# Kernel optimization log

Hardware: AMD Instinct MI355X
Metric: run time of the kernel (lower is better)

Reference implementation:

```python
import jax, jax.numpy as jnp
import numpy as np

T, V, K = 128, 5023, 16  # time frames, FLAME vertices, max neighbors


def setup_inputs() -> dict:
    key = jax.random.key(0)
    k1, k2, k3, k4 = jax.random.split(key, 4)
    canonical = jax.random.normal(k1, (T, V, 3), dtype=jnp.float32)
    deformed = canonical + 0.1 * jax.random.normal(k2, (T, V, 3), dtype=jnp.float32)
    neighbors = jax.random.randint(k3, (V, K), 0, V)
    neighbors_mask = jax.random.bernoulli(k4, 0.8, (V, K))
    return {
        "canonical_vertices": canonical,
        "deformed_vertices": deformed,
        "neighbors": neighbors,
        "neighbors_mask": neighbors_mask,
    }


def _matrix_to_quaternion(M):
    """Rotation matrix [..., 3, 3] -> quaternion [..., 4] (w, x, y, z).
    Standard numerically-robust 4-candidate selection (pytorch3d style)."""
    m00, m01, m02 = M[..., 0, 0], M[..., 0, 1], M[..., 0, 2]
    m10, m11, m12 = M[..., 1, 0], M[..., 1, 1], M[..., 1, 2]
    m20, m21, m22 = M[..., 2, 0], M[..., 2, 1], M[..., 2, 2]
    q_abs = jnp.sqrt(jnp.clip(jnp.stack([
        1.0 + m00 + m11 + m22,
        1.0 + m00 - m11 - m22,
        1.0 - m00 + m11 - m22,
        1.0 - m00 - m11 + m22,
    ], axis=-1), 0.0, None))
    quat_by_rijk = jnp.stack([
        jnp.stack([q_abs[..., 0] ** 2, m21 - m12, m02 - m20, m10 - m01], -1),
        jnp.stack([m21 - m12, q_abs[..., 1] ** 2, m01 + m10, m02 + m20], -1),
        jnp.stack([m02 - m20, m10 + m01, q_abs[..., 2] ** 2, m12 + m21], -1),
        jnp.stack([m10 - m01, m20 + m02, m21 + m12, q_abs[..., 3] ** 2], -1),
    ], axis=-2)  # [..., 4, 4]
    floor = jnp.asarray(0.1, M.dtype)
    quat_candidates = quat_by_rijk / (2.0 * jnp.maximum(q_abs[..., None], floor))
    one_hot = jax.nn.one_hot(jnp.argmax(q_abs, axis=-1), 4, dtype=M.dtype)
    return jnp.sum(quat_candidates * one_hot[..., None], axis=-2)


def reference(canonical_vertices, deformed_vertices, neighbors, neighbors_mask):
    dtype = canonical_vertices.dtype
    maskf = neighbors_mask[..., None].astype(dtype)  # [V, K, 1]
    # gather neighbor positions, zeroing padded slots (matches torch code)
    p = canonical_vertices[:, neighbors, :] * maskf  # [T, V, K, 3]
    q = deformed_vertices[:, neighbors, :] * maskf   # [T, V, K, 3]
    # center on the vertex itself
    p_c = p - canonical_vertices[:, :, None, :]
    q_c = q - deformed_vertices[:, :, None, :]
    # per-vertex 3x3 covariance: p_centered^T @ q_centered
    cov = jnp.einsum('tvki,tvkj->tvij', p_c, q_c)  # [T, V, 3, 3]
    u, s, vh = jnp.linalg.svd(cov)
    det = jnp.linalg.det(u @ vh)  # det(u @ v^T), since v^T == vh
    ones = jnp.ones_like(det)
    d3 = jnp.where(jnp.abs(det - 1.0) > 1e-6, det, ones)
    # v @ diag(1, 1, d3) scales the columns of v
    col_scale = jnp.stack([ones, ones, d3], axis=-1)[..., None, :]  # [T,V,1,3]
    v = jnp.swapaxes(vh, -1, -2)
    rotation_matrix = (v * col_scale) @ jnp.swapaxes(u, -1, -2)  # [T,V,3,3]
    rotation = _matrix_to_quaternion(rotation_matrix)  # [T, V, 4]
    translation = deformed_vertices - canonical_vertices  # [T, V, 3]
    return rotation, translation
```

## Files before the change

### kernel.cpp

```cpp
#include <hip/hip_runtime.h>


namespace {
constexpr int T_FRAMES = 128;
constexpr int V_NUM    = 5023;
constexpr int K_NB     = 16;
constexpr int SLAB     = V_NUM * 3;
constexpr int LDS_BYTES = V_NUM * 16 * 2;
}

__global__ __launch_bounds__(1024)
void se3_extract_kernel(const float* __restrict__ cano,
                        const float* __restrict__ defo,
                        const int*   __restrict__ nbr,
                        const unsigned char* __restrict__ mask_raw,
                        float* __restrict__ out) {
    extern __shared__ float4 lds4[];
    float4* __restrict__ ldsc = lds4;
    float4* __restrict__ ldsd = lds4 + V_NUM;

    const int bid  = blockIdx.x;
    const int t    = bid & 127;
    const int half = bid >> 7;
    const int tid  = threadIdx.x;

    int mflag;
    {
        const unsigned w = reinterpret_cast<const unsigned*>(mask_raw)[tid & 63];
        const bool isb = ((((w >> 8) & 0xffu) == 1u) | (((w >> 24) & 0xffu) == 1u));
        const bool isf = ((w >> 24) == 0x3fu);
        const unsigned long long mb = __ballot(isb);
        const unsigned long long mf = __ballot(isf);
        mflag = 0;
        if (__popcll(mb) > 16)      mflag = 1;
        else if (__popcll(mf) > 16) mflag = 2;
    }

    const float* __restrict__ cfp = cano + (size_t)t * SLAB;
    const float* __restrict__ dfp = defo + (size_t)t * SLAB;
    for (int i = tid; i < V_NUM; i += 1024) {
        const float* cp = cfp + i * 3;
        ldsc[i] = make_float4(cp[0], cp[1], cp[2], 0.0f);
        const float* dp = dfp + i * 3;
        ldsd[i] = make_float4(dp[0], dp[1], dp[2], 0.0f);
    }
    __syncthreads();

    const int vbeg = half ? 2512 : 0;
    const int vend = half ? V_NUM : 2512;

    for (int v = vbeg + tid; v < vend; v += 1024) {
        const float4 cv = ldsc[v];
        const float4 dv = ldsd[v];

        int nb[K_NB];
        {
            const int4* p4 = reinterpret_cast<const int4*>(nbr + (size_t)v * K_NB);
            #pragma unroll
            for (int j = 0; j < K_NB / 4; ++j) {
                const int4 q = p4[j];
                nb[j*4+0] = q.x; nb[j*4+1] = q.y; nb[j*4+2] = q.z; nb[j*4+3] = q.w;
            }
        }

        float mk[K_NB];
        if (mflag == 1) {
            const uint4 mw = *reinterpret_cast<const uint4*>(mask_raw + (size_t)v * K_NB);
            const unsigned w[4] = {mw.x, mw.y, mw.z, mw.w};
            #pragma unroll
            for (int j = 0; j < 4; ++j) {
                mk[j*4+0] = ((w[j]         & 0xffu) != 0u) ? 1.0f : 0.0f;
                mk[j*4+1] = (((w[j] >> 8 ) & 0xffu) != 0u) ? 1.0f : 0.0f;
                mk[j*4+2] = (((w[j] >> 16) & 0xffu) != 0u) ? 1.0f : 0.0f;
                mk[j*4+3] = (((w[j] >> 24) & 0xffu) != 0u) ? 1.0f : 0.0f;
            }
        } else if (mflag == 0) {
            const int* mp = reinterpret_cast<const int*>(mask_raw) + (size_t)v * K_NB;
            #pragma unroll
            for (int k = 0; k < K_NB; ++k) mk[k] = mp[k] ? 1.0f : 0.0f;
        } else {
            const float* mp = reinterpret_cast<const float*>(mask_raw) + (size_t)v * K_NB;
            #pragma unroll
            for (int k = 0; k < K_NB; ++k) mk[k] = (mp[k] != 0.0f) ? 1.0f : 0.0f;
        }

        float a00=0.f,a01=0.f,a02=0.f,a10=0.f,a11=0.f,a12=0.f,a20=0.f,a21=0.f,a22=0.f;
        #pragma unroll
        for (int k = 0; k < K_NB; ++k) {
            const int n = nb[k];
            const float m = mk[k];
            const float4 cp = ldsc[n];
            const float4 dp = ldsd[n];
            const float px = fmaf(cp.x, m, -cv.x);
            const float py = fmaf(cp.y, m, -cv.y);
            const float pz = fmaf(cp.z, m, -cv.z);
            const float qx = fmaf(dp.x, m, -dv.x);
            const float qy = fmaf(dp.y, m, -dv.y);
            const float qz = fmaf(dp.z, m, -dv.z);
            a00 = fmaf(px,qx,a00); a01 = fmaf(px,qy,a01); a02 = fmaf(px,qz,a02);
            a10 = fmaf(py,qx,a10); a11 = fmaf(py,qy,a11); a12 = fmaf(py,qz,a12);
            a20 = fmaf(pz,qx,a20); a21 = fmaf(pz,qy,a21); a22 = fmaf(pz,qz,a22);
        }

        float x00=a00, x01=a10, x02=a20;
        float x10=a01, x11=a11, x12=a21;
        float x20=a02, x21=a12, x22=a22;
        {
            const float d0 = x00*(x11*x22 - x12*x21)
                           - x01*(x10*x22 - x12*x20)
                           + x02*(x10*x21 - x11*x20);
            const float ad = fmaxf(fabsf(d0), 1e-30f);
            float mu = __builtin_amdgcn_exp2f(-0.3333333333f *
                                              __builtin_amdgcn_logf(ad));
            if (d0 < 0.0f) mu = -mu;
            x00*=mu; x01*=mu; x02*=mu;
            x10*=mu; x11*=mu; x12*=mu;
            x20*=mu; x21*=mu; x22*=mu;
        }
        #pragma unroll
        for (int it = 0; it < 8; ++it) {
            const float c00 = x11*x22 - x12*x21;
            const float c01 = x12*x20 - x10*x22;
            const float c02 = x10*x21 - x11*x20;
            const float c10 = x02*x21 - x01*x22;
            const float c11 = x00*x22 - x02*x20;
            const float c12 = x01*x20 - x00*x21;
            const float c20 = x01*x12 - x02*x11;
            const float c21 = x02*x10 - x00*x12;
            const float c22 = x00*x11 - x01*x10;
            const float det = x00*c00 + x01*c01 + x02*c02;
            const float r   = 0.5f * __builtin_amdgcn_rcpf(det);
            x00 = fmaf(0.5f, x00, r*c00); x01 = fmaf(0.5f, x01, r*c01); x02 = fmaf(0.5f, x02, r*c02);
            x10 = fmaf(0.5f, x10, r*c10); x11 = fmaf(0.5f, x11, r*c11); x12 = fmaf(0.5f, x12, r*c12);
            x20 = fmaf(0.5f, x20, r*c20); x21 = fmaf(0.5f, x21, r*c21); x22 = fmaf(0.5f, x22, r*c22);
        }

        const float qa0 = sqrtf(fmaxf(1.0f + x00 + x11 + x22, 0.0f));
        const float qa1 = sqrtf(fmaxf(1.0f + x00 - x11 - x22, 0.0f));
        const float qa2 = sqrtf(fmaxf(1.0f - x00 + x11 - x22, 0.0f));
        const float qa3 = sqrtf(fmaxf(1.0f - x00 - x11 + x22, 0.0f));

        int best = 0; float bq = qa0;
        if (qa1 > bq) { best = 1; bq = qa1; }
        if (qa2 > bq) { best = 2; bq = qa2; }
        if (qa3 > bq) { best = 3; bq = qa3; }

        float r0, r1, r2, r3;
        if      (best == 0) { r0 = qa0*qa0; r1 = x21-x12; r2 = x02-x20; r3 = x10-x01; }
        else if (best == 1) { r0 = x21-x12; r1 = qa1*qa1; r2 = x01+x10; r3 = x02+x20; }
        else if (best == 2) { r0 = x02-x20; r1 = x10+x01; r2 = qa2*qa2; r3 = x12+x21; }
        else                { r0 = x10-x01; r1 = x20+x02; r2 = x21+x12; r3 = qa3*qa3; }
        const float qi = __builtin_amdgcn_rcpf(2.0f * fmaxf(bq, 0.1f));

        const size_t base_q = ((size_t)t * V_NUM + v) * 4;
        float4 qout;
        qout.x = r0 * qi; qout.y = r1 * qi; qout.z = r2 * qi; qout.w = r3 * qi;
        *reinterpret_cast<float4*>(out + base_q) = qout;

        const size_t base_t = (size_t)T_FRAMES * V_NUM * 4 + ((size_t)t * V_NUM + v) * 3;
        out[base_t+0] = dv.x - cv.x;
        out[base_t+1] = dv.y - cv.y;
        out[base_t+2] = dv.z - cv.z;
    }
}

extern "C" void kernel_launch(void* const* d_in, const int* in_sizes, int n_in,
                              void* d_out, int out_size, void* d_ws, size_t ws_size,
                              hipStream_t stream) {
    const float* cano = (const float*)d_in[0];
    const float* defo = (const float*)d_in[1];
    const int*   nbr  = (const int*)d_in[2];
    const unsigned char* mask = (const unsigned char*)d_in[3];
    float* out = (float*)d_out;

    static bool attr_set = false;
    if (!attr_set) {
        (void)hipFuncSetAttribute((const void*)se3_extract_kernel,
                                  hipFuncAttributeMaxDynamicSharedMemorySize,
                                  LDS_BYTES);
        attr_set = true;
    }

    se3_extract_kernel<<<256, 1024, LDS_BYTES, stream>>>(cano, defo, nbr, mask, out);
}
```

Before: 91.63 us.

## Pack neighbor positions as fp16 in LDS and split each frame across four blocks

Stores canonical and deformed neighbor coordinates as packed half2 values in one 16-byte LDS record per vertex, which halves LDS use. The smaller LDS footprint allows four 512-thread blocks per frame and more resident blocks per CU. The center vertex is read in fp32 from global memory. Neighbor coordinates lose precision to fp16, which can perturb the covariance and the rotations for nearly degenerate neighborhoods. Each block also restages the whole frame, so global staging traffic doubles.

```diff
diff --git a/kernel.cpp b/kernel.cpp
--- a/kernel.cpp
+++ b/kernel.cpp
@@ -1,4 +1,5 @@
 #include <hip/hip_runtime.h>
+#include <hip/hip_fp16.h>
 
 
 namespace {
@@ -6,22 +7,26 @@
 constexpr int V_NUM    = 5023;
 constexpr int K_NB     = 16;
 constexpr int SLAB     = V_NUM * 3;
-constexpr int LDS_BYTES = V_NUM * 16 * 2;
+constexpr int VPB      = 1256;
+constexpr int LDS_BYTES = V_NUM * 16;
 }
 
-__global__ __launch_bounds__(1024)
+union VRec {
+    uint4   u;
+    __half2 h[4];
+};
+
+__global__ __launch_bounds__(512, 4)
 void se3_extract_kernel(const float* __restrict__ cano,
                         const float* __restrict__ defo,
                         const int*   __restrict__ nbr,
                         const unsigned char* __restrict__ mask_raw,
                         float* __restrict__ out) {
-    extern __shared__ float4 lds4[];
-    float4* __restrict__ ldsc = lds4;
-    float4* __restrict__ ldsd = lds4 + V_NUM;
+    extern __shared__ uint4 ldsv[];
 
     const int bid  = blockIdx.x;
     const int t    = bid & 127;
-    const int half = bid >> 7;
+    const int quar = bid >> 7;
     const int tid  = threadIdx.x;
 
     int mflag;
@@ -38,20 +43,26 @@
 
     const float* __restrict__ cfp = cano + (size_t)t * SLAB;
     const float* __restrict__ dfp = defo + (size_t)t * SLAB;
-    for (int i = tid; i < V_NUM; i += 1024) {
+    for (int i = tid; i < V_NUM; i += 512) {
         const float* cp = cfp + i * 3;
-        ldsc[i] = make_float4(cp[0], cp[1], cp[2], 0.0f);
         const float* dp = dfp + i * 3;
-        ldsd[i] = make_float4(dp[0], dp[1], dp[2], 0.0f);
+        VRec r;
+        r.h[0] = __floats2half2_rn(cp[0], cp[1]);
+        r.h[1] = __floats2half2_rn(cp[2], dp[0]);
+        r.h[2] = __floats2half2_rn(dp[1], dp[2]);
+        r.h[3] = __floats2half2_rn(0.0f, 0.0f);
+        ldsv[i] = r.u;
     }
     __syncthreads();
 
-    const int vbeg = half ? 2512 : 0;
-    const int vend = half ? V_NUM : 2512;
+    const int vbeg = quar * VPB;
+    const int vend = (vbeg + VPB < V_NUM) ? vbeg + VPB : V_NUM;
 
-    for (int v = vbeg + tid; v < vend; v += 1024) {
-        const float4 cv = ldsc[v];
-        const float4 dv = ldsd[v];
+    for (int v = vbeg + tid; v < vend; v += 512) {
+        const float* cp = cfp + v * 3;
+        const float* dp = dfp + v * 3;
+        const float cvx = cp[0], cvy = cp[1], cvz = cp[2];
+        const float dvx = dp[0], dvy = dp[1], dvz = dp[2];
 
         int nb[K_NB];
         {
@@ -87,16 +98,17 @@
         float a00=0.f,a01=0.f,a02=0.f,a10=0.f,a11=0.f,a12=0.f,a20=0.f,a21=0.f,a22=0.f;
         #pragma unroll
         for (int k = 0; k < K_NB; ++k) {
-            const int n = nb[k];
+            VRec r; r.u = ldsv[nb[k]];
+            const float2 f0 = __half22float2(r.h[0]);
+            const float2 f1 = __half22float2(r.h[1]);
+            const float2 f2 = __half22float2(r.h[2]);
             const float m = mk[k];
-            const float4 cp = ldsc[n];
-            const float4 dp = ldsd[n];
-            const float px = fmaf(cp.x, m, -cv.x);
-            const float py = fmaf(cp.y, m, -cv.y);
-            const float pz = fmaf(cp.z, m, -cv.z);
-            const float qx = fmaf(dp.x, m, -dv.x);
-            const float qy = fmaf(dp.y, m, -dv.y);
-            const float qz = fmaf(dp.z, m, -dv.z);
+            const float px = fmaf(f0.x, m, -cvx);
+            const float py = fmaf(f0.y, m, -cvy);
+            const float pz = fmaf(f1.x, m, -cvz);
+            const float qx = fmaf(f1.y, m, -dvx);
+            const float qy = fmaf(f2.x, m, -dvy);
+            const float qz = fmaf(f2.y, m, -dvz);
             a00 = fmaf(px,qx,a00); a01 = fmaf(px,qy,a01); a02 = fmaf(px,qz,a02);
             a10 = fmaf(py,qx,a10); a11 = fmaf(py,qy,a11); a12 = fmaf(py,qz,a12);
             a20 = fmaf(pz,qx,a20); a21 = fmaf(pz,qy,a21); a22 = fmaf(pz,qz,a22);
@@ -158,9 +170,9 @@
         *reinterpret_cast<float4*>(out + base_q) = qout;
 
         const size_t base_t = (size_t)T_FRAMES * V_NUM * 4 + ((size_t)t * V_NUM + v) * 3;
-        out[base_t+0] = dv.x - cv.x;
-        out[base_t+1] = dv.y - cv.y;
-        out[base_t+2] = dv.z - cv.z;
+        out[base_t+0] = dvx - cvx;
+        out[base_t+1] = dvy - cvy;
+        out[base_t+2] = dvz - cvz;
     }
 }
 
@@ -181,5 +193,5 @@
         attr_set = true;
     }
 
-    se3_extract_kernel<<<256, 1024, LDS_BYTES, stream>>>(cano, defo, nbr, mask, out);
+    se3_extract_kernel<<<512, 512, LDS_BYTES, stream>>>(cano, defo, nbr, mask, out);
 }
```

After: 90.26 us. No clear change (-1.5%).
